# Kernel optimization log

Measured on AMD Instinct MI355X. Metric: run time of the kernel, lower is better.

The kernel has to match this reference:

```python
import jax, jax.numpy as jnp
import numpy as np

NEG_SLOPE = 0.2  # PyG GATConv default negative_slope


def gat_conv(x, edge_index, W, att_src, att_dst, bias):
    """PyG-style GATConv (concat heads, add_self_loops=True, eval mode).
    x: [N, F_in], edge_index: [2, E] (row 0 = src j, row 1 = dst i).
    W: [F_in, H*C], att_src/att_dst: [H, C], bias: [H*C].
    """
    N = x.shape[0]
    H, C = att_src.shape
    loops = jnp.arange(N, dtype=edge_index.dtype)
    src = jnp.concatenate([edge_index[0], loops])  # [E+N]
    dst = jnp.concatenate([edge_index[1], loops])
    h = (x @ W).reshape(N, H, C)                              # [N,H,C]
    a_src = jnp.einsum('nhc,hc->nh', h, att_src)              # [N,H]
    a_dst = jnp.einsum('nhc,hc->nh', h, att_dst)
    alpha = jax.nn.leaky_relu(a_src[src] + a_dst[dst], NEG_SLOPE)  # [E+N,H]
    # segment softmax over edges sharing the same destination node
    m = jax.ops.segment_max(alpha, dst, num_segments=N)       # [N,H]
    e = jnp.exp(alpha - jax.lax.stop_gradient(m)[dst])
    denom = jax.ops.segment_sum(e, dst, num_segments=N)       # [N,H]
    a = e / (denom[dst] + 1e-16)                              # [E+N,H]
    msg = h[src] * a[:, :, None]                              # [E+N,H,C]
    out = jax.ops.segment_sum(msg, dst, num_segments=N)       # [N,H,C]
    return out.reshape(N, H * C) + bias


def setup_inputs() -> dict:
    key = jax.random.key(0)
    ks = jax.random.split(key, 10)
    N, F, NC, C1, H1 = 50000, 128, 40, 16, 8
    E = 800000
    x = jax.random.normal(ks[0], (N, F), dtype=jnp.float32)
    edge_index = jax.random.randint(ks[1], (2, E), 0, N, dtype=jnp.int64)
    s1 = 1.0 / np.sqrt(F)
    W1 = jax.random.uniform(ks[2], (F, H1 * C1), jnp.float32, -s1, s1)
    att_src1 = jax.random.uniform(ks[3], (H1, C1), jnp.float32, -1.0, 1.0) * s1
    att_dst1 = jax.random.uniform(ks[4], (H1, C1), jnp.float32, -1.0, 1.0) * s1
    bias1 = jnp.zeros((H1 * C1,), jnp.float32)
    s2 = 1.0 / np.sqrt(H1 * C1)
    W2 = jax.random.uniform(ks[5], (H1 * C1, NC), jnp.float32, -s2, s2)
    att_src2 = jax.random.uniform(ks[6], (1, NC), jnp.float32, -1.0, 1.0) * s2
    att_dst2 = jax.random.uniform(ks[7], (1, NC), jnp.float32, -1.0, 1.0) * s2
    bias2 = jnp.zeros((NC,), jnp.float32)
    return {"x": x, "edge_index": edge_index, "W1": W1, "att_src1": att_src1,
            "att_dst1": att_dst1, "bias1": bias1, "W2": W2, "att_src2": att_src2,
            "att_dst2": att_dst2, "bias2": bias2}


def reference(x, edge_index, W1, att_src1, att_dst1, bias1, W2, att_src2, att_dst2, bias2):
    h = gat_conv(x, edge_index, W1, att_src1, att_dst1, bias1)   # [N, 128]
    # dropout in eval mode = identity
    out = gat_conv(h, edge_index, W2, att_src2, att_dst2, bias2)  # [N, 40]
    return out
```

## Files before the change

kernel.cpp:

```cpp
#include <hip/hip_runtime.h>
#include <hip/hip_bf16.h>
#include <math.h>

#define NEG_SLOPE 0.2f

typedef __bf16 bf16x8 __attribute__((ext_vector_type(8)));
typedef float f32x4 __attribute__((ext_vector_type(4)));

__device__ __forceinline__ float lrelu(float x) { return x > 0.f ? x : NEG_SLOPE * x; }

__device__ __forceinline__ unsigned short f2bfu(float f) {
    unsigned int ua = __float_as_uint(f);
    return (unsigned short)((ua + 0x7fffu + ((ua >> 16) & 1u)) >> 16);
}
__device__ __forceinline__ float bfu2f(unsigned short u) {
    return __uint_as_float(((unsigned int)u) << 16);
}
__device__ __forceinline__ float bf_lo(unsigned int u) { return __uint_as_float(u << 16); }
__device__ __forceinline__ float bf_hi(unsigned int u) { return __uint_as_float(u & 0xffff0000u); }

__global__ __launch_bounds__(256) void k_prep(const float* __restrict__ W1,
                                              bf16x8* __restrict__ Wp,
                                              const float* __restrict__ W2,
                                              bf16x8* __restrict__ W2p,
                                              const float* __restrict__ att_s1,
                                              const float* __restrict__ att_d1,
                                              const float* __restrict__ att_s2,
                                              const float* __restrict__ att_d2,
                                              int* __restrict__ cnt, int N) {
    int g = blockIdx.x * 256 + threadIdx.x;
    if (g < 2048) {
        int n = g & 15, quad = (g >> 4) & 3, c = (g >> 6) & 3, ct = g >> 8;
        bf16x8 v;
#pragma unroll
        for (int j = 0; j < 8; ++j)
            v[j] = (__bf16)W1[(c * 32 + quad * 8 + j) * 128 + ct * 16 + n];
        Wp[g] = v;
    } else if (g < 2560) {
        int idx = g - 2048;
        int n = idx & 15, quad = (idx >> 4) & 3, c = (idx >> 6) & 3, t8 = idx >> 8;
        int h = n & 7;
        const float* av = (n < 8) ? att_s1 : att_d1;
        bf16x8 vv;
#pragma unroll
        for (int j = 0; j < 8; ++j) {
            int f = c * 32 + quad * 8 + j;
            float full = 0.f;
            for (int cc = 0; cc < 16; ++cc)
                full += W1[f * 128 + h * 16 + cc] * av[h * 16 + cc];
            __bf16 hi = (__bf16)full;
            vv[j] = t8 ? (__bf16)(full - (float)hi) : hi;
        }
        Wp[g] = vv;
    } else if (g < 3328) {
        int idx = g - 2560;
        int n = idx & 15, quad = (idx >> 4) & 3, c = (idx >> 6) & 3, ct = idx >> 8;
        int colc = ct * 16 + n;
        bf16x8 v;
        if (colc < 40) {
#pragma unroll
            for (int j = 0; j < 8; ++j)
                v[j] = (__bf16)W2[(c * 32 + quad * 8 + j) * 40 + colc];
        } else if (ct == 2 && n >= 8 && n < 12) {
            const float* av = (n & 1) ? att_d2 : att_s2;
#pragma unroll
            for (int j = 0; j < 8; ++j) {
                int f = c * 32 + quad * 8 + j;
                float full = 0.f;
                for (int cc = 0; cc < 40; ++cc) full += W2[f * 40 + cc] * av[cc];
                __bf16 hi = (__bf16)full;
                v[j] = (n >= 10) ? (__bf16)(full - (float)hi) : hi;
            }
        } else {
#pragma unroll
            for (int j = 0; j < 8; ++j) v[j] = (__bf16)0.f;
        }
        W2p[idx] = v;
    }
    if (g < N) cnt[g] = 0;
}

__global__ __launch_bounds__(256) void k_hist(const int* __restrict__ ei, int E, int N,
                                              int* __restrict__ cnt,
                                              unsigned short* __restrict__ rank) {
    int e = blockIdx.x * 256 + threadIdx.x;
    if (e >= E + N) return;
    int d = (e < E) ? ei[E + e] : (e - E);
    rank[e] = (unsigned short)atomicAdd(&cnt[d], 1);
}

__global__ __launch_bounds__(256) void k_scan_part(const int* __restrict__ cnt, int N,
                                                   int* __restrict__ psum) {
    __shared__ int sh[256];
    int t = threadIdx.x;
    int base = blockIdx.x * 1024 + t * 4;
    int tl = 0;
#pragma unroll
    for (int j = 0; j < 4; ++j) tl += (base + j < N) ? cnt[base + j] : 0;
    sh[t] = tl; __syncthreads();
    for (int off = 128; off > 0; off >>= 1) {
        if (t < off) sh[t] += sh[t + off];
        __syncthreads();
    }
    if (t == 0) psum[blockIdx.x] = sh[0];
}

__global__ __launch_bounds__(256) void k_scan_add(const int* __restrict__ cnt, int N,
                                                  const int* __restrict__ psum,
                                                  int* __restrict__ rowptr) {
    __shared__ int sh[256];
    __shared__ int basep;
    int t = threadIdx.x;
    if (t == 0) {
        int s = 0;
        for (int i = 0; i < blockIdx.x; ++i) s += psum[i];
        basep = s;
    }
    int base = blockIdx.x * 1024 + t * 4;
    int c[4]; int tl = 0;
#pragma unroll
    for (int j = 0; j < 4; ++j) { c[j] = (base + j < N) ? cnt[base + j] : 0; tl += c[j]; }
    sh[t] = tl; __syncthreads();
    for (int off = 1; off < 256; off <<= 1) {
        int a = (t >= off) ? sh[t - off] : 0;
        __syncthreads();
        sh[t] += a;
        __syncthreads();
    }
    int run = basep + (sh[t] - tl);
#pragma unroll
    for (int j = 0; j < 4; ++j) {
        if (base + j < N) { rowptr[base + j] = run; run += c[j]; }
    }
}

__global__ __launch_bounds__(256) void k_scatter(const int* __restrict__ ei, int E, int N,
                                                 const int* __restrict__ rowptr,
                                                 const unsigned short* __restrict__ rank,
                                                 unsigned short* __restrict__ col) {
    int e = blockIdx.x * 256 + threadIdx.x;
    if (e >= E + N) return;
    int s, d;
    if (e < E) { s = ei[e]; d = ei[E + e]; } else { s = d = e - E; }
    col[rowptr[d] + (int)rank[e]] = (unsigned short)s;
}

__global__ __launch_bounds__(256) void k_ev1(const int* __restrict__ rowptr,
                                             const unsigned short* __restrict__ col,
                                             const float* __restrict__ a_src,
                                             const float* __restrict__ a_dst,
                                             float* __restrict__ evA,
                                             float* __restrict__ evB,
                                             unsigned short* __restrict__ d16,
                                             int N, int EN) {
    int slot = blockIdx.x * 256 + threadIdx.x;
    if (slot >= EN) return;
    int lo = 0, hi = N - 1;
    while (lo < hi) {
        int mid = (lo + hi + 1) >> 1;
        if (rowptr[mid] <= slot) lo = mid; else hi = mid - 1;
    }
    int d = lo;
    int s = (int)col[slot];
    d16[slot] = (unsigned short)d;
    float4 asA = *(const float4*)&a_src[(size_t)s * 8];
    float4 asB = *(const float4*)&a_src[(size_t)s * 8 + 4];
    float4 adA = *(const float4*)&a_dst[(size_t)d * 8];
    float4 adB = *(const float4*)&a_dst[(size_t)d * 8 + 4];
    float4 eA = make_float4(__expf(lrelu(asA.x + adA.x)), __expf(lrelu(asA.y + adA.y)),
                            __expf(lrelu(asA.z + adA.z)), __expf(lrelu(asA.w + adA.w)));
    float4 eB = make_float4(__expf(lrelu(asB.x + adB.x)), __expf(lrelu(asB.y + adB.y)),
                            __expf(lrelu(asB.z + adB.z)), __expf(lrelu(asB.w + adB.w)));
    *(float4*)&evA[(size_t)slot * 4] = eA;
    *(float4*)&evB[(size_t)slot * 4] = eB;
}

__global__ __launch_bounds__(256) void k_ev2(const unsigned short* __restrict__ col,
                                             const unsigned short* __restrict__ d16,
                                             const float* __restrict__ a_src2,
                                             const float* __restrict__ a_dst2,
                                             float* __restrict__ ev2, int EN) {
    int slot = blockIdx.x * 256 + threadIdx.x;
    if (slot >= EN) return;
    int s = (int)col[slot];
    int d = (int)d16[slot];
    ev2[slot] = __expf(lrelu(a_src2[s] + a_dst2[d]));
}

__global__ __launch_bounds__(256) void k_gemm1(const float* __restrict__ x,
                                               const bf16x8* __restrict__ Wp,
                                               unsigned short* __restrict__ h1A,
                                               unsigned short* __restrict__ h1B,
                                               float* __restrict__ a_src,
                                               float* __restrict__ a_dst, int N) {
    int t = threadIdx.x;
    int w = t >> 6, lane = t & 63, quad = lane >> 4, n16 = lane & 15;
    int row0 = blockIdx.x * 64 + w * 16;
    int arow = row0 + n16; if (arow >= N) arow = N - 1;
    const float* px = x + (size_t)arow * 128;

    bf16x8 ah[4], al[4];
#pragma unroll
    for (int c = 0; c < 4; ++c) {
        float4 v0 = *(const float4*)&px[c * 32 + quad * 8];
        float4 v1 = *(const float4*)&px[c * 32 + quad * 8 + 4];
        float xf[8] = {v0.x, v0.y, v0.z, v0.w, v1.x, v1.y, v1.z, v1.w};
#pragma unroll
        for (int j = 0; j < 8; ++j) {
            __bf16 hi = (__bf16)xf[j];
            ah[c][j] = hi;
            al[c][j] = (__bf16)(xf[j] - (float)hi);
        }
    }

    f32x4 acc[10];
#pragma unroll
    for (int ct = 0; ct < 10; ++ct) acc[ct] = (f32x4){0.f, 0.f, 0.f, 0.f};

    const uint4* wp4 = (const uint4*)Wp;
#pragma unroll
    for (int ct = 0; ct < 10; ++ct) {
#pragma unroll
        for (int c = 0; c < 4; ++c) {
            union { uint4 u; bf16x8 b; } bu;
            bu.u = wp4[((ct * 4 + c) * 4 + quad) * 16 + n16];
            acc[ct] = __builtin_amdgcn_mfma_f32_16x16x32_bf16(ah[c], bu.b, acc[ct], 0, 0, 0);
            acc[ct] = __builtin_amdgcn_mfma_f32_16x16x32_bf16(al[c], bu.b, acc[ct], 0, 0, 0);
        }
    }

    int nodeb = row0 + quad * 4;
#pragma unroll
    for (int ct = 0; ct < 8; ++ct) {
        unsigned short* hp = (ct < 4) ? h1A : h1B;
        int chl = (ct & 3) * 16 + n16;
#pragma unroll
        for (int reg = 0; reg < 4; ++reg) {
            int node = nodeb + reg;
            if (node < N) hp[(size_t)node * 64 + chl] = f2bfu(acc[ct][reg]);
        }
    }
#pragma unroll
    for (int reg = 0; reg < 4; ++reg) {
        int node = nodeb + reg;
        float av = acc[8][reg] + acc[9][reg];
        if (node < N) {
            if (n16 < 8) a_src[(size_t)node * 8 + n16] = av;
            else         a_dst[(size_t)node * 8 + (n16 - 8)] = av;
        }
    }
}

__global__ __launch_bounds__(256) void k_aggr1(const int* __restrict__ rowptr,
                                               const int* __restrict__ cnt,
                                               const unsigned short* __restrict__ col,
                                               const float* __restrict__ evA,
                                               const float* __restrict__ evB,
                                               const unsigned int* __restrict__ h1A,
                                               const unsigned int* __restrict__ h1B,
                                               const float* __restrict__ bias1,
                                               unsigned int* __restrict__ out1h,
                                               unsigned int* __restrict__ out1l,
                                               int N, int nag) {
    __shared__ float evs[4][2][128];
    __shared__ int   cls[4][2][32];
    int p = (blockIdx.x >= nag) ? 1 : 0;
    int blk = blockIdx.x - p * nag;
    const uint4* hp4 = (const uint4*)(p ? h1B : h1A);
    const float4* evp = (const float4*)(p ? evB : evA);
    int t = threadIdx.x;
    int w = t >> 6;
    int lane = t & 63;
    int half = lane >> 5;
    int u = lane & 31;
    int e4 = u >> 3;
    int v  = u & 7;
    int hh = v >> 1;
    int node = blk * 8 + w * 2 + half;
    bool nv = (node < N);
    int nodec = nv ? node : (N - 1);
    int beg = rowptr[nodec];
    int deg = nv ? cnt[nodec] : 0;
    int degO = __shfl_xor(deg, 32);
    int degmax = (deg > degO) ? deg : degO;
    if (degmax <= 0) return;

    float* myev = &evs[w][half][0];
    int*   mycl = &cls[w][half][0];

    float den = 0.f;
    float nm[8];
#pragma unroll
    for (int k = 0; k < 8; ++k) nm[k] = 0.f;

    int c = 0;
    while (c < degmax) {
        int slot = c + u;
        int slotc = (slot < deg) ? slot : (deg - 1);
        if (slotc < 0) slotc = 0;
        int su = (int)col[beg + slotc];
        float4 e4v = evp[beg + slotc];
        if (slot >= deg) e4v = make_float4(0.f, 0.f, 0.f, 0.f);
        *(float4*)&myev[u * 4] = e4v;
        mycl[u] = su;

        int ccm = degmax - c; ccm = (ccm < 32) ? ccm : 32;
        int ng = (ccm + 3) >> 2;
        int gl = ng - 1;
        int g1 = (1 < gl) ? 1 : gl;
        int g2 = (2 < gl) ? 2 : gl;
        int g3 = (3 < gl) ? 3 : gl;
        uint4 U0 = hp4[mycl[e4] * 8 + v];
        uint4 U1 = hp4[mycl[g1 * 4 + e4] * 8 + v];
        uint4 U2 = hp4[mycl[g2 * 4 + e4] * 8 + v];
        uint4 U3 = hp4[mycl[g3 * 4 + e4] * 8 + v];
        int body = ng - 4;
        int g = 0;
#pragma unroll 2
        for (; g < body; ++g) {
            uint4 UN = hp4[mycl[(g + 4) * 4 + e4] * 8 + v];
            float ev = myev[(g * 4 + e4) * 4 + hh];
            den += ev;
            nm[0] = fmaf(ev, bf_lo(U0.x), nm[0]);
            nm[1] = fmaf(ev, bf_hi(U0.x), nm[1]);
            nm[2] = fmaf(ev, bf_lo(U0.y), nm[2]);
            nm[3] = fmaf(ev, bf_hi(U0.y), nm[3]);
            nm[4] = fmaf(ev, bf_lo(U0.z), nm[4]);
            nm[5] = fmaf(ev, bf_hi(U0.z), nm[5]);
            nm[6] = fmaf(ev, bf_lo(U0.w), nm[6]);
            nm[7] = fmaf(ev, bf_hi(U0.w), nm[7]);
            U0 = U1; U1 = U2; U2 = U3; U3 = UN;
        }
        for (; g < ng; ++g) {
            float ev = myev[(g * 4 + e4) * 4 + hh];
            den += ev;
            nm[0] = fmaf(ev, bf_lo(U0.x), nm[0]);
            nm[1] = fmaf(ev, bf_hi(U0.x), nm[1]);
            nm[2] = fmaf(ev, bf_lo(U0.y), nm[2]);
            nm[3] = fmaf(ev, bf_hi(U0.y), nm[3]);
            nm[4] = fmaf(ev, bf_lo(U0.z), nm[4]);
            nm[5] = fmaf(ev, bf_hi(U0.z), nm[5]);
            nm[6] = fmaf(ev, bf_lo(U0.w), nm[6]);
            nm[7] = fmaf(ev, bf_hi(U0.w), nm[7]);
            U0 = U1; U1 = U2; U2 = U3;
        }
        c += 32;
    }
    den += __shfl_xor(den, 8);
    den += __shfl_xor(den, 16);
#pragma unroll
    for (int k = 0; k < 8; ++k) {
        nm[k] += __shfl_xor(nm[k], 8);
        nm[k] += __shfl_xor(nm[k], 16);
    }
    if (nv && e4 == 0) {
        float inv = 1.f / (den + 1e-16f);
        float4 b0 = *(const float4*)&bias1[p * 64 + v * 8];
        float4 b1 = *(const float4*)&bias1[p * 64 + v * 8 + 4];
        float bb[8] = {b0.x, b0.y, b0.z, b0.w, b1.x, b1.y, b1.z, b1.w};
        unsigned int H[4], L[4];
#pragma unroll
        for (int q = 0; q < 4; ++q) {
            float o0 = fmaf(nm[2 * q],     inv, bb[2 * q]);
            float o1 = fmaf(nm[2 * q + 1], inv, bb[2 * q + 1]);
            unsigned short h0 = f2bfu(o0), h1 = f2bfu(o1);
            float l0 = o0 - bfu2f(h0), l1 = o1 - bfu2f(h1);
            H[q] = (unsigned int)h0 | ((unsigned int)h1 << 16);
            L[q] = (unsigned int)f2bfu(l0) | ((unsigned int)f2bfu(l1) << 16);
        }
        size_t idx = (size_t)node * 64 + p * 32 + v * 4;
        *(uint4*)&out1h[idx] = make_uint4(H[0], H[1], H[2], H[3]);
        *(uint4*)&out1l[idx] = make_uint4(L[0], L[1], L[2], L[3]);
    }
}

__global__ __launch_bounds__(256) void k_gemm2(const unsigned int* __restrict__ out1h,
                                               const unsigned int* __restrict__ out1l,
                                               const bf16x8* __restrict__ W2p,
                                               unsigned short* __restrict__ h2s,
                                               float* __restrict__ a_src2,
                                               float* __restrict__ a_dst2, int N) {
    int t = threadIdx.x;
    int w = t >> 6, lane = t & 63, quad = lane >> 4, n16 = lane & 15;
    int row0 = blockIdx.x * 64 + w * 16;
    int arow = row0 + n16; if (arow >= N) arow = N - 1;

    bf16x8 ah[4], al[4];
#pragma unroll
    for (int c = 0; c < 4; ++c) {
        size_t base = (size_t)arow * 64 + (c * 32 + quad * 8) / 2;
        union { uint4 u; bf16x8 b; } hu, lu;
        hu.u = *(const uint4*)&out1h[base];
        lu.u = *(const uint4*)&out1l[base];
        ah[c] = hu.b;
        al[c] = lu.b;
    }

    f32x4 acc[3];
#pragma unroll
    for (int ct = 0; ct < 3; ++ct) acc[ct] = (f32x4){0.f, 0.f, 0.f, 0.f};

    const uint4* wp4 = (const uint4*)W2p;
#pragma unroll
    for (int ct = 0; ct < 3; ++ct) {
#pragma unroll
        for (int c = 0; c < 4; ++c) {
            union { uint4 u; bf16x8 b; } bu;
            bu.u = wp4[((ct * 4 + c) * 4 + quad) * 16 + n16];
            acc[ct] = __builtin_amdgcn_mfma_f32_16x16x32_bf16(ah[c], bu.b, acc[ct], 0, 0, 0);
            acc[ct] = __builtin_amdgcn_mfma_f32_16x16x32_bf16(al[c], bu.b, acc[ct], 0, 0, 0);
        }
    }

    int nodeb = row0 + quad * 4;
#pragma unroll
    for (int reg = 0; reg < 4; ++reg) {
        int node = nodeb + reg;
#pragma unroll
        for (int ct = 0; ct < 3; ++ct) {
            int ch = ct * 16 + n16;
            if (node < N && ch < 40) h2s[(size_t)node * 64 + ch] = f2bfu(acc[ct][reg]);
        }
        float fv = acc[2][reg];
        float fused = fv + __shfl_xor(fv, 2);
        if (node < N) {
            if (n16 == 8) a_src2[node] = fused;
            else if (n16 == 9) a_dst2[node] = fused;
        }
    }
}

__global__ __launch_bounds__(256) void k_aggr2(const int* __restrict__ rowptr,
                                               const int* __restrict__ cnt,
                                               const unsigned short* __restrict__ col,
                                               const float* __restrict__ ev2,
                                               const unsigned int* __restrict__ h2b,
                                               const float* __restrict__ bias2,
                                               float* __restrict__ out, int N) {
    __shared__ float evs[4][2][32];
    __shared__ int   cls[4][2][32];
    int t = threadIdx.x;
    int w = t >> 6;
    int lane = t & 63;
    int half = lane >> 5;
    int u = lane & 31;
    int e4 = u >> 3;
    int v  = u & 7;
    int node = blockIdx.x * 8 + w * 2 + half;
    bool nv = (node < N);
    int nodec = nv ? node : (N - 1);
    int beg = rowptr[nodec];
    int deg = nv ? cnt[nodec] : 0;
    int degO = __shfl_xor(deg, 32);
    int degmax = (deg > degO) ? deg : degO;
    if (degmax <= 0) return;

    const uint4* h24 = (const uint4*)h2b;
    float* myev = &evs[w][half][0];
    int*   mycl = &cls[w][half][0];

    float den = 0.f;
    float am[8];
#pragma unroll
    for (int k = 0; k < 8; ++k) am[k] = 0.f;

    int c = 0;
    while (c < degmax) {
        int slot = c + u;
        int slotc = (slot < deg) ? slot : (deg - 1);
        if (slotc < 0) slotc = 0;
        int su = (int)col[beg + slotc];
        float ev = ev2[beg + slotc];
        if (slot >= deg) ev = 0.f;
        myev[u] = ev;
        mycl[u] = su;

        int ccm = degmax - c; ccm = (ccm < 32) ? ccm : 32;
        int ng = (ccm + 3) >> 2;
        int gl = ng - 1;
        int g1 = (1 < gl) ? 1 : gl;
        int g2 = (2 < gl) ? 2 : gl;
        int g3 = (3 < gl) ? 3 : gl;
        uint4 U0 = h24[mycl[e4] * 8 + v];
        uint4 U1 = h24[mycl[g1 * 4 + e4] * 8 + v];
        uint4 U2 = h24[mycl[g2 * 4 + e4] * 8 + v];
        uint4 U3 = h24[mycl[g3 * 4 + e4] * 8 + v];
        int body = ng - 4;
        int g = 0;
#pragma unroll 2
        for (; g < body; ++g) {
            uint4 UN = h24[mycl[(g + 4) * 4 + e4] * 8 + v];
            float evv = myev[g * 4 + e4];
            den += evv;
            am[0] = fmaf(evv, bf_lo(U0.x), am[0]);
            am[1] = fmaf(evv, bf_hi(U0.x), am[1]);
            am[2] = fmaf(evv, bf_lo(U0.y), am[2]);
            am[3] = fmaf(evv, bf_hi(U0.y), am[3]);
            am[4] = fmaf(evv, bf_lo(U0.z), am[4]);
            am[5] = fmaf(evv, bf_hi(U0.z), am[5]);
            am[6] = fmaf(evv, bf_lo(U0.w), am[6]);
            am[7] = fmaf(evv, bf_hi(U0.w), am[7]);
            U0 = U1; U1 = U2; U2 = U3; U3 = UN;
        }
        for (; g < ng; ++g) {
            float evv = myev[g * 4 + e4];
            den += evv;
            am[0] = fmaf(evv, bf_lo(U0.x), am[0]);
            am[1] = fmaf(evv, bf_hi(U0.x), am[1]);
            am[2] = fmaf(evv, bf_lo(U0.y), am[2]);
            am[3] = fmaf(evv, bf_hi(U0.y), am[3]);
            am[4] = fmaf(evv, bf_lo(U0.z), am[4]);
            am[5] = fmaf(evv, bf_hi(U0.z), am[5]);
            am[6] = fmaf(evv, bf_lo(U0.w), am[6]);
            am[7] = fmaf(evv, bf_hi(U0.w), am[7]);
            U0 = U1; U1 = U2; U2 = U3;
        }
        c += 32;
    }
    den += __shfl_xor(den, 8);
    den += __shfl_xor(den, 16);
#pragma unroll
    for (int k = 0; k < 8; ++k) {
        am[k] += __shfl_xor(am[k], 8);
        am[k] += __shfl_xor(am[k], 16);
    }
    if (nv && e4 == 0 && v < 5) {
        float inv = 1.f / (den + 1e-16f);
        float4 b0 = *(const float4*)&bias2[v * 8];
        float4 b1 = *(const float4*)&bias2[v * 8 + 4];
        float4 o0 = make_float4(fmaf(am[0], inv, b0.x), fmaf(am[1], inv, b0.y),
                                fmaf(am[2], inv, b0.z), fmaf(am[3], inv, b0.w));
        float4 o1 = make_float4(fmaf(am[4], inv, b1.x), fmaf(am[5], inv, b1.y),
                                fmaf(am[6], inv, b1.z), fmaf(am[7], inv, b1.w));
        size_t ob = (size_t)node * 40 + v * 8;
        *(float4*)&out[ob] = o0;
        *(float4*)&out[ob + 4] = o1;
    }
}

extern "C" void kernel_launch(void* const* d_in, const int* in_sizes, int n_in,
                              void* d_out, int out_size, void* d_ws, size_t ws_size,
                              hipStream_t stream) {
    const float* x   = (const float*)d_in[0];
    const int*   ei  = (const int*)d_in[1];
    const float* W1  = (const float*)d_in[2];
    const float* as1 = (const float*)d_in[3];
    const float* ad1 = (const float*)d_in[4];
    const float* b1  = (const float*)d_in[5];
    const float* W2  = (const float*)d_in[6];
    const float* as2 = (const float*)d_in[7];
    const float* ad2 = (const float*)d_in[8];
    const float* b2  = (const float*)d_in[9];

    int N = in_sizes[0] / 128;
    int E = in_sizes[1] / 2;
    int EN = E + N;
    size_t Np = (size_t)((N + 3) & ~3);
    size_t ENp = ((size_t)EN + 3) & ~3;

    float* ws = (float*)d_ws;
    unsigned int* out1h = (unsigned int*)ws; ws += Np * 64;
    unsigned int* out1l = (unsigned int*)ws; ws += Np * 64;
    unsigned int* h1A = (unsigned int*)ws; ws += Np * 32;
    unsigned int* h1Bp = (unsigned int*)ws; ws += Np * 32;
    unsigned int* h2b = (unsigned int*)ws; ws += Np * 32;
    float* a_src1  = ws; ws += Np * 8;
    float* a_dst1  = ws; ws += Np * 8;
    float* a_src2v = ws; ws += Np;
    float* a_dst2v = ws; ws += Np;
    float* evA = ws; ws += ENp * 4;
    float* evB = ws; ws += ENp * 4;
    float* ev2 = ws; ws += ENp;
    bf16x8* Wp  = (bf16x8*)ws; ws += 2560 * 4;
    bf16x8* W2p = (bf16x8*)ws; ws += 768 * 4;
    int* cnt    = (int*)ws; ws += Np;
    int* rowptr = (int*)ws; ws += Np;
    int* psum   = (int*)ws; ws += 256;
    unsigned short* col  = (unsigned short*)ws; ws += ENp / 2 + 4;
    unsigned short* rank = (unsigned short*)ws; ws += ENp / 2 + 4;
    unsigned short* d16  = (unsigned short*)ws; ws += ENp / 2 + 4;

    int nb = (N + 1023) / 1024;
    int npre = (N > 3328 ? N : 3328);

    k_prep<<<(npre + 255) / 256, 256, 0, stream>>>(W1, Wp, W2, W2p,
                                                   as1, ad1, as2, ad2, cnt, N);
    k_hist<<<(EN + 255) / 256, 256, 0, stream>>>(ei, E, N, cnt, rank);
    k_scan_part<<<nb, 256, 0, stream>>>(cnt, N, psum);
    k_scan_add<<<nb, 256, 0, stream>>>(cnt, N, psum, rowptr);
    k_scatter<<<(EN + 255) / 256, 256, 0, stream>>>(ei, E, N, rowptr, rank, col);

    k_gemm1<<<(N + 63) / 64, 256, 0, stream>>>(x, Wp,
                                               (unsigned short*)h1A, (unsigned short*)h1Bp,
                                               a_src1, a_dst1, N);
    k_ev1<<<(EN + 255) / 256, 256, 0, stream>>>(rowptr, col, a_src1, a_dst1,
                                                evA, evB, d16, N, EN);
    int nag = (N + 7) / 8;
    k_aggr1<<<2 * nag, 256, 0, stream>>>(rowptr, cnt, col, evA, evB,
                                         h1A, h1Bp, b1, out1h, out1l, N, nag);
    k_gemm2<<<(N + 63) / 64, 256, 0, stream>>>(out1h, out1l, W2p,
                                               (unsigned short*)h2b, a_src2v, a_dst2v, N);
    k_ev2<<<(EN + 255) / 256, 256, 0, stream>>>(col, d16, a_src2v, a_dst2v, ev2, EN);
    k_aggr2<<<nag, 256, 0, stream>>>(rowptr, cnt, col, ev2, h2b, b2, (float*)d_out, N);
}
```

Measured before the change: 245.2 us.

## Fuse edge attention computation into aggregation kernels with block-level edge windows

```diff
diff --git a/kernel.cpp b/kernel.cpp
--- a/kernel.cpp
+++ b/kernel.cpp
@@ -3,6 +3,7 @@
 #include <math.h>
 
 #define NEG_SLOPE 0.2f
+#define WSZ 512
 
 typedef __bf16 bf16x8 __attribute__((ext_vector_type(8)));
 typedef float f32x4 __attribute__((ext_vector_type(4)));
@@ -130,7 +131,10 @@
     int run = basep + (sh[t] - tl);
 #pragma unroll
     for (int j = 0; j < 4; ++j) {
-        if (base + j < N) { rowptr[base + j] = run; run += c[j]; }
+        if (base + j < N) {
+            rowptr[base + j] = run; run += c[j];
+            if (base + j == N - 1) rowptr[N] = run;
+        }
     }
 }
 
@@ -143,48 +147,6 @@
     int s, d;
     if (e < E) { s = ei[e]; d = ei[E + e]; } else { s = d = e - E; }
     col[rowptr[d] + (int)rank[e]] = (unsigned short)s;
-}
-
-__global__ __launch_bounds__(256) void k_ev1(const int* __restrict__ rowptr,
-                                             const unsigned short* __restrict__ col,
-                                             const float* __restrict__ a_src,
-                                             const float* __restrict__ a_dst,
-                                             float* __restrict__ evA,
-                                             float* __restrict__ evB,
-                                             unsigned short* __restrict__ d16,
-                                             int N, int EN) {
-    int slot = blockIdx.x * 256 + threadIdx.x;
-    if (slot >= EN) return;
-    int lo = 0, hi = N - 1;
-    while (lo < hi) {
-        int mid = (lo + hi + 1) >> 1;
-        if (rowptr[mid] <= slot) lo = mid; else hi = mid - 1;
-    }
-    int d = lo;
-    int s = (int)col[slot];
-    d16[slot] = (unsigned short)d;
-    float4 asA = *(const float4*)&a_src[(size_t)s * 8];
-    float4 asB = *(const float4*)&a_src[(size_t)s * 8 + 4];
-    float4 adA = *(const float4*)&a_dst[(size_t)d * 8];
-    float4 adB = *(const float4*)&a_dst[(size_t)d * 8 + 4];
-    float4 eA = make_float4(__expf(lrelu(asA.x + adA.x)), __expf(lrelu(asA.y + adA.y)),
-                            __expf(lrelu(asA.z + adA.z)), __expf(lrelu(asA.w + adA.w)));
-    float4 eB = make_float4(__expf(lrelu(asB.x + adB.x)), __expf(lrelu(asB.y + adB.y)),
-                            __expf(lrelu(asB.z + adB.z)), __expf(lrelu(asB.w + adB.w)));
-    *(float4*)&evA[(size_t)slot * 4] = eA;
-    *(float4*)&evB[(size_t)slot * 4] = eB;
-}
-
-__global__ __launch_bounds__(256) void k_ev2(const unsigned short* __restrict__ col,
-                                             const unsigned short* __restrict__ d16,
-                                             const float* __restrict__ a_src2,
-                                             const float* __restrict__ a_dst2,
-                                             float* __restrict__ ev2, int EN) {
-    int slot = blockIdx.x * 256 + threadIdx.x;
-    if (slot >= EN) return;
-    int s = (int)col[slot];
-    int d = (int)d16[slot];
-    ev2[slot] = __expf(lrelu(a_src2[s] + a_dst2[d]));
 }
 
 __global__ __launch_bounds__(256) void k_gemm1(const float* __restrict__ x,
@@ -252,99 +214,122 @@
 }
 
 __global__ __launch_bounds__(256) void k_aggr1(const int* __restrict__ rowptr,
-                                               const int* __restrict__ cnt,
                                                const unsigned short* __restrict__ col,
-                                               const float* __restrict__ evA,
-                                               const float* __restrict__ evB,
+                                               const float* __restrict__ a_src,
+                                               const float* __restrict__ a_dst,
                                                const unsigned int* __restrict__ h1A,
                                                const unsigned int* __restrict__ h1B,
                                                const float* __restrict__ bias1,
                                                unsigned int* __restrict__ out1h,
                                                unsigned int* __restrict__ out1l,
                                                int N, int nag) {
-    __shared__ float evs[4][2][128];
-    __shared__ int   cls[4][2][32];
+    __shared__ float4 evL[WSZ];
+    __shared__ int    colL[WSZ];
+    __shared__ int    rpL[9];
+    __shared__ float4 adL[8];
     int p = (blockIdx.x >= nag) ? 1 : 0;
     int blk = blockIdx.x - p * nag;
     const uint4* hp4 = (const uint4*)(p ? h1B : h1A);
-    const float4* evp = (const float4*)(p ? evB : evA);
     int t = threadIdx.x;
-    int w = t >> 6;
-    int lane = t & 63;
-    int half = lane >> 5;
-    int u = lane & 31;
-    int e4 = u >> 3;
-    int v  = u & 7;
-    int hh = v >> 1;
-    int node = blk * 8 + w * 2 + half;
+    int node0 = blk * 8;
+    if (t < 9) {
+        int nd = node0 + t; if (nd > N) nd = N;
+        rpL[t] = rowptr[nd];
+    }
+    if (t >= 64 && t < 72) {
+        int nd = node0 + (t - 64); if (nd >= N) nd = N - 1;
+        adL[t - 64] = *(const float4*)&a_dst[(size_t)nd * 8 + p * 4];
+    }
+    __syncthreads();
+    int w0v = rpL[0], end8 = rpL[8];
+
+    int w = t >> 6, lane = t & 63, half = lane >> 5, u = lane & 31;
+    int e4 = u >> 3, v = u & 7, hh = v >> 1;
+    int idx8 = w * 2 + half;
+    int node = node0 + idx8;
     bool nv = (node < N);
-    int nodec = nv ? node : (N - 1);
-    int beg = rowptr[nodec];
-    int deg = nv ? cnt[nodec] : 0;
-    int degO = __shfl_xor(deg, 32);
-    int degmax = (deg > degO) ? deg : degO;
-    if (degmax <= 0) return;
-
-    float* myev = &evs[w][half][0];
-    int*   mycl = &cls[w][half][0];
+    int beg = rpL[idx8], end = rpL[idx8 + 1];
 
     float den = 0.f;
     float nm[8];
 #pragma unroll
     for (int k = 0; k < 8; ++k) nm[k] = 0.f;
 
-    int c = 0;
-    while (c < degmax) {
-        int slot = c + u;
-        int slotc = (slot < deg) ? slot : (deg - 1);
-        if (slotc < 0) slotc = 0;
-        int su = (int)col[beg + slotc];
-        float4 e4v = evp[beg + slotc];
-        if (slot >= deg) e4v = make_float4(0.f, 0.f, 0.f, 0.f);
-        *(float4*)&myev[u * 4] = e4v;
-        mycl[u] = su;
-
-        int ccm = degmax - c; ccm = (ccm < 32) ? ccm : 32;
-        int ng = (ccm + 3) >> 2;
-        int gl = ng - 1;
-        int g1 = (1 < gl) ? 1 : gl;
-        int g2 = (2 < gl) ? 2 : gl;
-        int g3 = (3 < gl) ? 3 : gl;
-        uint4 U0 = hp4[mycl[e4] * 8 + v];
-        uint4 U1 = hp4[mycl[g1 * 4 + e4] * 8 + v];
-        uint4 U2 = hp4[mycl[g2 * 4 + e4] * 8 + v];
-        uint4 U3 = hp4[mycl[g3 * 4 + e4] * 8 + v];
-        int body = ng - 4;
-        int g = 0;
+    for (int w0 = w0v; w0 < end8; w0 += WSZ) {
+        int wend = w0 + WSZ; if (wend > end8) wend = end8;
+        int wsz = wend - w0;
+        if (w0 != w0v) __syncthreads();
+        for (int s = w0 + t; s < wend; s += 256) {
+            int su = (int)col[s];
+            int lo2 = 0;
+            if (rpL[lo2 + 4] <= s) lo2 += 4;
+            if (rpL[lo2 + 2] <= s) lo2 += 2;
+            if (rpL[lo2 + 1] <= s) lo2 += 1;
+            float4 as4 = *(const float4*)&a_src[(size_t)su * 8 + p * 4];
+            float4 ad4 = adL[lo2];
+            float4 e;
+            e.x = __expf(lrelu(as4.x + ad4.x));
+            e.y = __expf(lrelu(as4.y + ad4.y));
+            e.z = __expf(lrelu(as4.z + ad4.z));
+            e.w = __expf(lrelu(as4.w + ad4.w));
+            evL[s - w0] = e;
+            colL[s - w0] = su;
+        }
+        __syncthreads();
+        int lbeg = (beg > w0) ? beg : w0;
+        int lend = (end < wend) ? end : wend;
+        int ldeg = lend - lbeg;
+        int ldO = __shfl_xor(ldeg, 32);
+        int ldm = (ldeg > ldO) ? ldeg : ldO;
+        int ob0 = lbeg - w0;
+        const float* evf = (const float*)evL;
+        for (int c = 0; c < ldm; c += 32) {
+            int ccm = ldeg - c; ccm = (ccm < 32) ? ccm : 32;
+            int ng = (ccm + 3) >> 2;
+            int gl = ng - 1;
+            int g1 = (1 < gl) ? 1 : gl;
+            int g2 = (2 < gl) ? 2 : gl;
+            int g3 = (3 < gl) ? 3 : gl;
+            int ob = ob0 + c;
+#define CIDX(i) ({ int _x = ob + (i); _x = (_x < 0) ? 0 : _x; (_x >= wsz) ? (wsz - 1) : _x; })
+            uint4 U0 = hp4[colL[CIDX(e4)] * 8 + v];
+            uint4 U1 = hp4[colL[CIDX(g1 * 4 + e4)] * 8 + v];
+            uint4 U2 = hp4[colL[CIDX(g2 * 4 + e4)] * 8 + v];
+            uint4 U3 = hp4[colL[CIDX(g3 * 4 + e4)] * 8 + v];
+            int body = ng - 4;
+            int g = 0;
 #pragma unroll 2
-        for (; g < body; ++g) {
-            uint4 UN = hp4[mycl[(g + 4) * 4 + e4] * 8 + v];
-            float ev = myev[(g * 4 + e4) * 4 + hh];
-            den += ev;
-            nm[0] = fmaf(ev, bf_lo(U0.x), nm[0]);
-            nm[1] = fmaf(ev, bf_hi(U0.x), nm[1]);
-            nm[2] = fmaf(ev, bf_lo(U0.y), nm[2]);
-            nm[3] = fmaf(ev, bf_hi(U0.y), nm[3]);
-            nm[4] = fmaf(ev, bf_lo(U0.z), nm[4]);
-            nm[5] = fmaf(ev, bf_hi(U0.z), nm[5]);
-            nm[6] = fmaf(ev, bf_lo(U0.w), nm[6]);
-            nm[7] = fmaf(ev, bf_hi(U0.w), nm[7]);
-            U0 = U1; U1 = U2; U2 = U3; U3 = UN;
-        }
-        for (; g < ng; ++g) {
-            float ev = myev[(g * 4 + e4) * 4 + hh];
-            den += ev;
-            nm[0] = fmaf(ev, bf_lo(U0.x), nm[0]);
-            nm[1] = fmaf(ev, bf_hi(U0.x), nm[1]);
-            nm[2] = fmaf(ev, bf_lo(U0.y), nm[2]);
-            nm[3] = fmaf(ev, bf_hi(U0.y), nm[3]);
-            nm[4] = fmaf(ev, bf_lo(U0.z), nm[4]);
-            nm[5] = fmaf(ev, bf_hi(U0.z), nm[5]);
-            nm[6] = fmaf(ev, bf_lo(U0.w), nm[6]);
-            nm[7] = fmaf(ev, bf_hi(U0.w), nm[7]);
-            U0 = U1; U1 = U2; U2 = U3;
-        }
-        c += 32;
+            for (; g < body; ++g) {
+                uint4 UN = hp4[colL[CIDX((g + 4) * 4 + e4)] * 8 + v];
+                int ii = g * 4 + e4;
+                float ev = (c + ii < ldeg) ? evf[CIDX(ii) * 4 + hh] : 0.f;
+                den += ev;
+                nm[0] = fmaf(ev, bf_lo(U0.x), nm[0]);
+                nm[1] = fmaf(ev, bf_hi(U0.x), nm[1]);
+                nm[2] = fmaf(ev, bf_lo(U0.y), nm[2]);
+                nm[3] = fmaf(ev, bf_hi(U0.y), nm[3]);
+                nm[4] = fmaf(ev, bf_lo(U0.z), nm[4]);
+                nm[5] = fmaf(ev, bf_hi(U0.z), nm[5]);
+                nm[6] = fmaf(ev, bf_lo(U0.w), nm[6]);
+                nm[7] = fmaf(ev, bf_hi(U0.w), nm[7]);
+                U0 = U1; U1 = U2; U2 = U3; U3 = UN;
+            }
+            for (; g < ng; ++g) {
+                int ii = g * 4 + e4;
+                float ev = (c + ii < ldeg) ? evf[CIDX(ii) * 4 + hh] : 0.f;
+                den += ev;
+                nm[0] = fmaf(ev, bf_lo(U0.x), nm[0]);
+                nm[1] = fmaf(ev, bf_hi(U0.x), nm[1]);
+                nm[2] = fmaf(ev, bf_lo(U0.y), nm[2]);
+                nm[3] = fmaf(ev, bf_hi(U0.y), nm[3]);
+                nm[4] = fmaf(ev, bf_lo(U0.z), nm[4]);
+                nm[5] = fmaf(ev, bf_hi(U0.z), nm[5]);
+                nm[6] = fmaf(ev, bf_lo(U0.w), nm[6]);
+                nm[7] = fmaf(ev, bf_hi(U0.w), nm[7]);
+                U0 = U1; U1 = U2; U2 = U3;
+            }
+#undef CIDX
+        }
     }
     den += __shfl_xor(den, 8);
     den += __shfl_xor(den, 16);
@@ -431,91 +416,109 @@
 }
 
 __global__ __launch_bounds__(256) void k_aggr2(const int* __restrict__ rowptr,
-                                               const int* __restrict__ cnt,
                                                const unsigned short* __restrict__ col,
-                                               const float* __restrict__ ev2,
+                                               const float* __restrict__ a_src2,
+                                               const float* __restrict__ a_dst2,
                                                const unsigned int* __restrict__ h2b,
                                                const float* __restrict__ bias2,
                                                float* __restrict__ out, int N) {
-    __shared__ float evs[4][2][32];
-    __shared__ int   cls[4][2][32];
+    __shared__ float evL[WSZ];
+    __shared__ int   colL[WSZ];
+    __shared__ int   rpL[9];
+    __shared__ float adL[8];
     int t = threadIdx.x;
-    int w = t >> 6;
-    int lane = t & 63;
-    int half = lane >> 5;
-    int u = lane & 31;
-    int e4 = u >> 3;
-    int v  = u & 7;
-    int node = blockIdx.x * 8 + w * 2 + half;
+    int node0 = blockIdx.x * 8;
+    if (t < 9) {
+        int nd = node0 + t; if (nd > N) nd = N;
+        rpL[t] = rowptr[nd];
+    }
+    if (t >= 64 && t < 72) {
+        int nd = node0 + (t - 64); if (nd >= N) nd = N - 1;
+        adL[t - 64] = a_dst2[nd];
+    }
+    __syncthreads();
+    int w0v = rpL[0], end8 = rpL[8];
+
+    int w = t >> 6, lane = t & 63, half = lane >> 5, u = lane & 31;
+    int e4 = u >> 3, v = u & 7;
+    int idx8 = w * 2 + half;
+    int node = node0 + idx8;
     bool nv = (node < N);
-    int nodec = nv ? node : (N - 1);
-    int beg = rowptr[nodec];
-    int deg = nv ? cnt[nodec] : 0;
-    int degO = __shfl_xor(deg, 32);
-    int degmax = (deg > degO) ? deg : degO;
-    if (degmax <= 0) return;
+    int beg = rpL[idx8], end = rpL[idx8 + 1];
 
     const uint4* h24 = (const uint4*)h2b;
-    float* myev = &evs[w][half][0];
-    int*   mycl = &cls[w][half][0];
-
     float den = 0.f;
     float am[8];
 #pragma unroll
     for (int k = 0; k < 8; ++k) am[k] = 0.f;
 
-    int c = 0;
-    while (c < degmax) {
-        int slot = c + u;
-        int slotc = (slot < deg) ? slot : (deg - 1);
-        if (slotc < 0) slotc = 0;
-        int su = (int)col[beg + slotc];
-        float ev = ev2[beg + slotc];
-        if (slot >= deg) ev = 0.f;
-        myev[u] = ev;
-        mycl[u] = su;
-
-        int ccm = degmax - c; ccm = (ccm < 32) ? ccm : 32;
-        int ng = (ccm + 3) >> 2;
-        int gl = ng - 1;
-        int g1 = (1 < gl) ? 1 : gl;
-        int g2 = (2 < gl) ? 2 : gl;
-        int g3 = (3 < gl) ? 3 : gl;
-        uint4 U0 = h24[mycl[e4] * 8 + v];
-        uint4 U1 = h24[mycl[g1 * 4 + e4] * 8 + v];
-        uint4 U2 = h24[mycl[g2 * 4 + e4] * 8 + v];
-        uint4 U3 = h24[mycl[g3 * 4 + e4] * 8 + v];
-        int body = ng - 4;
-        int g = 0;
+    for (int w0 = w0v; w0 < end8; w0 += WSZ) {
+        int wend = w0 + WSZ; if (wend > end8) wend = end8;
+        int wsz = wend - w0;
+        if (w0 != w0v) __syncthreads();
+        for (int s = w0 + t; s < wend; s += 256) {
+            int su = (int)col[s];
+            int lo2 = 0;
+            if (rpL[lo2 + 4] <= s) lo2 += 4;
+            if (rpL[lo2 + 2] <= s) lo2 += 2;
+            if (rpL[lo2 + 1] <= s) lo2 += 1;
+            evL[s - w0] = __expf(lrelu(a_src2[su] + adL[lo2]));
+            colL[s - w0] = su;
+        }
+        __syncthreads();
+        int lbeg = (beg > w0) ? beg : w0;
+        int lend = (end < wend) ? end : wend;
+        int ldeg = lend - lbeg;
+        int ldO = __shfl_xor(ldeg, 32);
+        int ldm = (ldeg > ldO) ? ldeg : ldO;
+        int ob0 = lbeg - w0;
+        for (int c = 0; c < ldm; c += 32) {
+            int ccm = ldeg - c; ccm = (ccm < 32) ? ccm : 32;
+            int ng = (ccm + 3) >> 2;
+            int gl = ng - 1;
+            int g1 = (1 < gl) ? 1 : gl;
+            int g2 = (2 < gl) ? 2 : gl;
+            int g3 = (3 < gl) ? 3 : gl;
+            int ob = ob0 + c;
+#define CIDX(i) ({ int _x = ob + (i); _x = (_x < 0) ? 0 : _x; (_x >= wsz) ? (wsz - 1) : _x; })
+            uint4 U0 = h24[colL[CIDX(e4)] * 8 + v];
+            uint4 U1 = h24[colL[CIDX(g1 * 4 + e4)] * 8 + v];
+            uint4 U2 = h24[colL[CIDX(g2 * 4 + e4)] * 8 + v];
+            uint4 U3 = h24[colL[CIDX(g3 * 4 + e4)] * 8 + v];
+            int body = ng - 4;
+            int g = 0;
 #pragma unroll 2
-        for (; g < body; ++g) {
-            uint4 UN = h24[mycl[(g + 4) * 4 + e4] * 8 + v];
-            float evv = myev[g * 4 + e4];
-            den += evv;
-            am[0] = fmaf(evv, bf_lo(U0.x), am[0]);
-            am[1] = fmaf(evv, bf_hi(U0.x), am[1]);
-            am[2] = fmaf(evv, bf_lo(U0.y), am[2]);
-            am[3] = fmaf(evv, bf_hi(U0.y), am[3]);
-            am[4] = fmaf(evv, bf_lo(U0.z), am[4]);
-            am[5] = fmaf(evv, bf_hi(U0.z), am[5]);
-            am[6] = fmaf(evv, bf_lo(U0.w), am[6]);
-            am[7] = fmaf(evv, bf_hi(U0.w), am[7]);
-            U0 = U1; U1 = U2; U2 = U3; U3 = UN;
-        }
-        for (; g < ng; ++g) {
-            float evv = myev[g * 4 + e4];
-            den += evv;
-            am[0] = fmaf(evv, bf_lo(U0.x), am[0]);
-            am[1] = fmaf(evv, bf_hi(U0.x), am[1]);
-            am[2] = fmaf(evv, bf_lo(U0.y), am[2]);
-            am[3] = fmaf(evv, bf_hi(U0.y), am[3]);
-            am[4] = fmaf(evv, bf_lo(U0.z), am[4]);
-            am[5] = fmaf(evv, bf_hi(U0.z), am[5]);
-            am[6] = fmaf(evv, bf_lo(U0.w), am[6]);
-            am[7] = fmaf(evv, bf_hi(U0.w), am[7]);
-            U0 = U1; U1 = U2; U2 = U3;
-        }
-        c += 32;
+            for (; g < body; ++g) {
+                uint4 UN = h24[colL[CIDX((g + 4) * 4 + e4)] * 8 + v];
+                int ii = g * 4 + e4;
+                float evv = (c + ii < ldeg) ? evL[CIDX(ii)] : 0.f;
+                den += evv;
+                am[0] = fmaf(evv, bf_lo(U0.x), am[0]);
+                am[1] = fmaf(evv, bf_hi(U0.x), am[1]);
+                am[2] = fmaf(evv, bf_lo(U0.y), am[2]);
+                am[3] = fmaf(evv, bf_hi(U0.y), am[3]);
+                am[4] = fmaf(evv, bf_lo(U0.z), am[4]);
+                am[5] = fmaf(evv, bf_hi(U0.z), am[5]);
+                am[6] = fmaf(evv, bf_lo(U0.w), am[6]);
+                am[7] = fmaf(evv, bf_hi(U0.w), am[7]);
+                U0 = U1; U1 = U2; U2 = U3; U3 = UN;
+            }
+            for (; g < ng; ++g) {
+                int ii = g * 4 + e4;
+                float evv = (c + ii < ldeg) ? evL[CIDX(ii)] : 0.f;
+                den += evv;
+                am[0] = fmaf(evv, bf_lo(U0.x), am[0]);
+                am[1] = fmaf(evv, bf_hi(U0.x), am[1]);
+                am[2] = fmaf(evv, bf_lo(U0.y), am[2]);
+                am[3] = fmaf(evv, bf_hi(U0.y), am[3]);
+                am[4] = fmaf(evv, bf_lo(U0.z), am[4]);
+                am[5] = fmaf(evv, bf_hi(U0.z), am[5]);
+                am[6] = fmaf(evv, bf_lo(U0.w), am[6]);
+                am[7] = fmaf(evv, bf_hi(U0.w), am[7]);
+                U0 = U1; U1 = U2; U2 = U3;
+            }
+#undef CIDX
+        }
     }
     den += __shfl_xor(den, 8);
     den += __shfl_xor(den, 16);
@@ -568,38 +571,31 @@
     float* a_dst1  = ws; ws += Np * 8;
     float* a_src2v = ws; ws += Np;
     float* a_dst2v = ws; ws += Np;
-    float* evA = ws; ws += ENp * 4;
-    float* evB = ws; ws += ENp * 4;
-    float* ev2 = ws; ws += ENp;
     bf16x8* Wp  = (bf16x8*)ws; ws += 2560 * 4;
     bf16x8* W2p = (bf16x8*)ws; ws += 768 * 4;
     int* cnt    = (int*)ws; ws += Np;
-    int* rowptr = (int*)ws; ws += Np;
+    int* rowptr = (int*)ws; ws += Np + 4;
     int* psum   = (int*)ws; ws += 256;
     unsigned short* col  = (unsigned short*)ws; ws += ENp / 2 + 4;
     unsigned short* rank = (unsigned short*)ws; ws += ENp / 2 + 4;
-    unsigned short* d16  = (unsigned short*)ws; ws += ENp / 2 + 4;
 
     int nb = (N + 1023) / 1024;
     int npre = (N > 3328 ? N : 3328);
 
     k_prep<<<(npre + 255) / 256, 256, 0, stream>>>(W1, Wp, W2, W2p,
                                                    as1, ad1, as2, ad2, cnt, N);
+    k_gemm1<<<(N + 63) / 64, 256, 0, stream>>>(x, Wp,
+                                               (unsigned short*)h1A, (unsigned short*)h1Bp,
+                                               a_src1, a_dst1, N);
     k_hist<<<(EN + 255) / 256, 256, 0, stream>>>(ei, E, N, cnt, rank);
     k_scan_part<<<nb, 256, 0, stream>>>(cnt, N, psum);
     k_scan_add<<<nb, 256, 0, stream>>>(cnt, N, psum, rowptr);
     k_scatter<<<(EN + 255) / 256, 256, 0, stream>>>(ei, E, N, rowptr, rank, col);
 
-    k_gemm1<<<(N + 63) / 64, 256, 0, stream>>>(x, Wp,
-                                               (unsigned short*)h1A, (unsigned short*)h1Bp,
-                                               a_src1, a_dst1, N);
-    k_ev1<<<(EN + 255) / 256, 256, 0, stream>>>(rowptr, col, a_src1, a_dst1,
-                                                evA, evB, d16, N, EN);
     int nag = (N + 7) / 8;
-    k_aggr1<<<2 * nag, 256, 0, stream>>>(rowptr, cnt, col, evA, evB,
+    k_aggr1<<<2 * nag, 256, 0, stream>>>(rowptr, col, a_src1, a_dst1,
                                          h1A, h1Bp, b1, out1h, out1l, N, nag);
     k_gemm2<<<(N + 63) / 64, 256, 0, stream>>>(out1h, out1l, W2p,
                                                (unsigned short*)h2b, a_src2v, a_dst2v, N);
-    k_ev2<<<(EN + 255) / 256, 256, 0, stream>>>(col, d16, a_src2v, a_dst2v, ev2, EN);
-    k_aggr2<<<nag, 256, 0, stream>>>(rowptr, cnt, col, ev2, h2b, b2, (float*)d_out, N);
-}
+    k_aggr2<<<nag, 256, 0, stream>>>(rowptr, col, a_src2v, a_dst2v, h2b, b2, (float*)d_out, N);
+}
```

Result: faster. 235.8 us (-3.8%).

## Fuse edge-score computation into aggregation kernels and restructure aggr1 per-lane gather

Applied to the files above, without the earlier changes.

```diff
diff --git a/kernel.cpp b/kernel.cpp
--- a/kernel.cpp
+++ b/kernel.cpp
@@ -145,48 +145,6 @@
     col[rowptr[d] + (int)rank[e]] = (unsigned short)s;
 }
 
-__global__ __launch_bounds__(256) void k_ev1(const int* __restrict__ rowptr,
-                                             const unsigned short* __restrict__ col,
-                                             const float* __restrict__ a_src,
-                                             const float* __restrict__ a_dst,
-                                             float* __restrict__ evA,
-                                             float* __restrict__ evB,
-                                             unsigned short* __restrict__ d16,
-                                             int N, int EN) {
-    int slot = blockIdx.x * 256 + threadIdx.x;
-    if (slot >= EN) return;
-    int lo = 0, hi = N - 1;
-    while (lo < hi) {
-        int mid = (lo + hi + 1) >> 1;
-        if (rowptr[mid] <= slot) lo = mid; else hi = mid - 1;
-    }
-    int d = lo;
-    int s = (int)col[slot];
-    d16[slot] = (unsigned short)d;
-    float4 asA = *(const float4*)&a_src[(size_t)s * 8];
-    float4 asB = *(const float4*)&a_src[(size_t)s * 8 + 4];
-    float4 adA = *(const float4*)&a_dst[(size_t)d * 8];
-    float4 adB = *(const float4*)&a_dst[(size_t)d * 8 + 4];
-    float4 eA = make_float4(__expf(lrelu(asA.x + adA.x)), __expf(lrelu(asA.y + adA.y)),
-                            __expf(lrelu(asA.z + adA.z)), __expf(lrelu(asA.w + adA.w)));
-    float4 eB = make_float4(__expf(lrelu(asB.x + adB.x)), __expf(lrelu(asB.y + adB.y)),
-                            __expf(lrelu(asB.z + adB.z)), __expf(lrelu(asB.w + adB.w)));
-    *(float4*)&evA[(size_t)slot * 4] = eA;
-    *(float4*)&evB[(size_t)slot * 4] = eB;
-}
-
-__global__ __launch_bounds__(256) void k_ev2(const unsigned short* __restrict__ col,
-                                             const unsigned short* __restrict__ d16,
-                                             const float* __restrict__ a_src2,
-                                             const float* __restrict__ a_dst2,
-                                             float* __restrict__ ev2, int EN) {
-    int slot = blockIdx.x * 256 + threadIdx.x;
-    if (slot >= EN) return;
-    int s = (int)col[slot];
-    int d = (int)d16[slot];
-    ev2[slot] = __expf(lrelu(a_src2[s] + a_dst2[d]));
-}
-
 __global__ __launch_bounds__(256) void k_gemm1(const float* __restrict__ x,
                                                const bf16x8* __restrict__ Wp,
                                                unsigned short* __restrict__ h1A,
@@ -254,8 +212,8 @@
 __global__ __launch_bounds__(256) void k_aggr1(const int* __restrict__ rowptr,
                                                const int* __restrict__ cnt,
                                                const unsigned short* __restrict__ col,
-                                               const float* __restrict__ evA,
-                                               const float* __restrict__ evB,
+                                               const float* __restrict__ a_src,
+                                               const float* __restrict__ a_dst,
                                                const unsigned int* __restrict__ h1A,
                                                const unsigned int* __restrict__ h1B,
                                                const float* __restrict__ bias1,
@@ -266,16 +224,12 @@
     __shared__ int   cls[4][2][32];
     int p = (blockIdx.x >= nag) ? 1 : 0;
     int blk = blockIdx.x - p * nag;
-    const uint4* hp4 = (const uint4*)(p ? h1B : h1A);
-    const float4* evp = (const float4*)(p ? evB : evA);
+    const unsigned int* hp = p ? h1B : h1A;
     int t = threadIdx.x;
     int w = t >> 6;
     int lane = t & 63;
     int half = lane >> 5;
     int u = lane & 31;
-    int e4 = u >> 3;
-    int v  = u & 7;
-    int hh = v >> 1;
     int node = blk * 8 + w * 2 + half;
     bool nv = (node < N);
     int nodec = nv ? node : (N - 1);
@@ -285,92 +239,69 @@
     int degmax = (deg > degO) ? deg : degO;
     if (degmax <= 0) return;
 
+    int hh = u >> 3;
+    float4 ad4 = *(const float4*)&a_dst[(size_t)nodec * 8 + p * 4];
+
     float* myev = &evs[w][half][0];
     int*   mycl = &cls[w][half][0];
 
-    float den = 0.f;
-    float nm[8];
-#pragma unroll
-    for (int k = 0; k < 8; ++k) nm[k] = 0.f;
-
+    float den = 0.f, n0 = 0.f, n1 = 0.f;
     int c = 0;
     while (c < degmax) {
         int slot = c + u;
         int slotc = (slot < deg) ? slot : (deg - 1);
         if (slotc < 0) slotc = 0;
         int su = (int)col[beg + slotc];
-        float4 e4v = evp[beg + slotc];
-        if (slot >= deg) e4v = make_float4(0.f, 0.f, 0.f, 0.f);
-        *(float4*)&myev[u * 4] = e4v;
+        float4 as4 = *(const float4*)&a_src[(size_t)su * 8 + p * 4];
+        bool valid = (slot < deg);
+        float e0 = valid ? __expf(lrelu(as4.x + ad4.x)) : 0.f;
+        float e1 = valid ? __expf(lrelu(as4.y + ad4.y)) : 0.f;
+        float e2 = valid ? __expf(lrelu(as4.z + ad4.z)) : 0.f;
+        float e3 = valid ? __expf(lrelu(as4.w + ad4.w)) : 0.f;
+        *(float4*)&myev[u * 4] = make_float4(e0, e1, e2, e3);
         mycl[u] = su;
 
         int ccm = degmax - c; ccm = (ccm < 32) ? ccm : 32;
-        int ng = (ccm + 3) >> 2;
-        int gl = ng - 1;
-        int g1 = (1 < gl) ? 1 : gl;
-        int g2 = (2 < gl) ? 2 : gl;
-        int g3 = (3 < gl) ? 3 : gl;
-        uint4 U0 = hp4[mycl[e4] * 8 + v];
-        uint4 U1 = hp4[mycl[g1 * 4 + e4] * 8 + v];
-        uint4 U2 = hp4[mycl[g2 * 4 + e4] * 8 + v];
-        uint4 U3 = hp4[mycl[g3 * 4 + e4] * 8 + v];
-        int body = ng - 4;
-        int g = 0;
-#pragma unroll 2
-        for (; g < body; ++g) {
-            uint4 UN = hp4[mycl[(g + 4) * 4 + e4] * 8 + v];
-            float ev = myev[(g * 4 + e4) * 4 + hh];
+        int last = ccm - 1;
+        int s0 = mycl[0];
+        unsigned int u0 = hp[s0 * 32 + u];
+        int i1 = (1 < last) ? 1 : last;
+        int s1 = mycl[i1];
+        unsigned int u1 = hp[s1 * 32 + u];
+        int i2 = (2 < last) ? 2 : last;
+        int s2 = mycl[i2];
+        unsigned int u2 = hp[s2 * 32 + u];
+        int body = ccm - 3;
+        int i = 0;
+#pragma unroll 4
+        for (; i < body; ++i) {
+            int sN = mycl[i + 3];
+            unsigned int uN = hp[sN * 32 + u];
+            float ev = myev[i * 4 + hh];
             den += ev;
-            nm[0] = fmaf(ev, bf_lo(U0.x), nm[0]);
-            nm[1] = fmaf(ev, bf_hi(U0.x), nm[1]);
-            nm[2] = fmaf(ev, bf_lo(U0.y), nm[2]);
-            nm[3] = fmaf(ev, bf_hi(U0.y), nm[3]);
-            nm[4] = fmaf(ev, bf_lo(U0.z), nm[4]);
-            nm[5] = fmaf(ev, bf_hi(U0.z), nm[5]);
-            nm[6] = fmaf(ev, bf_lo(U0.w), nm[6]);
-            nm[7] = fmaf(ev, bf_hi(U0.w), nm[7]);
-            U0 = U1; U1 = U2; U2 = U3; U3 = UN;
-        }
-        for (; g < ng; ++g) {
-            float ev = myev[(g * 4 + e4) * 4 + hh];
+            n0 = fmaf(ev, bf_lo(u0), n0);
+            n1 = fmaf(ev, bf_hi(u0), n1);
+            u0 = u1; u1 = u2; u2 = uN;
+        }
+        for (; i < ccm; ++i) {
+            float ev = myev[i * 4 + hh];
             den += ev;
-            nm[0] = fmaf(ev, bf_lo(U0.x), nm[0]);
-            nm[1] = fmaf(ev, bf_hi(U0.x), nm[1]);
-            nm[2] = fmaf(ev, bf_lo(U0.y), nm[2]);
-            nm[3] = fmaf(ev, bf_hi(U0.y), nm[3]);
-            nm[4] = fmaf(ev, bf_lo(U0.z), nm[4]);
-            nm[5] = fmaf(ev, bf_hi(U0.z), nm[5]);
-            nm[6] = fmaf(ev, bf_lo(U0.w), nm[6]);
-            nm[7] = fmaf(ev, bf_hi(U0.w), nm[7]);
-            U0 = U1; U1 = U2; U2 = U3;
+            n0 = fmaf(ev, bf_lo(u0), n0);
+            n1 = fmaf(ev, bf_hi(u0), n1);
+            u0 = u1; u1 = u2;
         }
         c += 32;
     }
-    den += __shfl_xor(den, 8);
-    den += __shfl_xor(den, 16);
-#pragma unroll
-    for (int k = 0; k < 8; ++k) {
-        nm[k] += __shfl_xor(nm[k], 8);
-        nm[k] += __shfl_xor(nm[k], 16);
-    }
-    if (nv && e4 == 0) {
+    if (nv) {
         float inv = 1.f / (den + 1e-16f);
-        float4 b0 = *(const float4*)&bias1[p * 64 + v * 8];
-        float4 b1 = *(const float4*)&bias1[p * 64 + v * 8 + 4];
-        float bb[8] = {b0.x, b0.y, b0.z, b0.w, b1.x, b1.y, b1.z, b1.w};
-        unsigned int H[4], L[4];
-#pragma unroll
-        for (int q = 0; q < 4; ++q) {
-            float o0 = fmaf(nm[2 * q],     inv, bb[2 * q]);
-            float o1 = fmaf(nm[2 * q + 1], inv, bb[2 * q + 1]);
-            unsigned short h0 = f2bfu(o0), h1 = f2bfu(o1);
-            float l0 = o0 - bfu2f(h0), l1 = o1 - bfu2f(h1);
-            H[q] = (unsigned int)h0 | ((unsigned int)h1 << 16);
-            L[q] = (unsigned int)f2bfu(l0) | ((unsigned int)f2bfu(l1) << 16);
-        }
-        size_t idx = (size_t)node * 64 + p * 32 + v * 4;
-        *(uint4*)&out1h[idx] = make_uint4(H[0], H[1], H[2], H[3]);
-        *(uint4*)&out1l[idx] = make_uint4(L[0], L[1], L[2], L[3]);
+        int ch = p * 64 + 2 * u;
+        float2 b = *(const float2*)&bias1[ch];
+        float o0 = fmaf(n0, inv, b.x), o1 = fmaf(n1, inv, b.y);
+        unsigned short h0 = f2bfu(o0), h1 = f2bfu(o1);
+        float l0 = o0 - bfu2f(h0), l1 = o1 - bfu2f(h1);
+        size_t idx = (size_t)node * 64 + p * 32 + u;
+        out1h[idx] = (unsigned int)h0 | ((unsigned int)h1 << 16);
+        out1l[idx] = (unsigned int)f2bfu(l0) | ((unsigned int)f2bfu(l1) << 16);
     }
 }
 
@@ -433,7 +364,8 @@
 __global__ __launch_bounds__(256) void k_aggr2(const int* __restrict__ rowptr,
                                                const int* __restrict__ cnt,
                                                const unsigned short* __restrict__ col,
-                                               const float* __restrict__ ev2,
+                                               const float* __restrict__ a_src,
+                                               const float* __restrict__ a_dst,
                                                const unsigned int* __restrict__ h2b,
                                                const float* __restrict__ bias2,
                                                float* __restrict__ out, int N) {
@@ -456,6 +388,7 @@
     if (degmax <= 0) return;
 
     const uint4* h24 = (const uint4*)h2b;
+    float ad = a_dst[nodec];
     float* myev = &evs[w][half][0];
     int*   mycl = &cls[w][half][0];
 
@@ -470,8 +403,7 @@
         int slotc = (slot < deg) ? slot : (deg - 1);
         if (slotc < 0) slotc = 0;
         int su = (int)col[beg + slotc];
-        float ev = ev2[beg + slotc];
-        if (slot >= deg) ev = 0.f;
+        float ev = (slot < deg) ? __expf(lrelu(a_src[su] + ad)) : 0.f;
         myev[u] = ev;
         mycl[u] = su;
 
@@ -568,38 +500,31 @@
     float* a_dst1  = ws; ws += Np * 8;
     float* a_src2v = ws; ws += Np;
     float* a_dst2v = ws; ws += Np;
-    float* evA = ws; ws += ENp * 4;
-    float* evB = ws; ws += ENp * 4;
-    float* ev2 = ws; ws += ENp;
     bf16x8* Wp  = (bf16x8*)ws; ws += 2560 * 4;
     bf16x8* W2p = (bf16x8*)ws; ws += 768 * 4;
     int* cnt    = (int*)ws; ws += Np;
-    int* rowptr = (int*)ws; ws += Np;
+    int* rowptr = (int*)ws; ws += Np + 4;
     int* psum   = (int*)ws; ws += 256;
     unsigned short* col  = (unsigned short*)ws; ws += ENp / 2 + 4;
     unsigned short* rank = (unsigned short*)ws; ws += ENp / 2 + 4;
-    unsigned short* d16  = (unsigned short*)ws; ws += ENp / 2 + 4;
 
     int nb = (N + 1023) / 1024;
     int npre = (N > 3328 ? N : 3328);
 
     k_prep<<<(npre + 255) / 256, 256, 0, stream>>>(W1, Wp, W2, W2p,
                                                    as1, ad1, as2, ad2, cnt, N);
+    k_gemm1<<<(N + 63) / 64, 256, 0, stream>>>(x, Wp,
+                                               (unsigned short*)h1A, (unsigned short*)h1Bp,
+                                               a_src1, a_dst1, N);
     k_hist<<<(EN + 255) / 256, 256, 0, stream>>>(ei, E, N, cnt, rank);
     k_scan_part<<<nb, 256, 0, stream>>>(cnt, N, psum);
     k_scan_add<<<nb, 256, 0, stream>>>(cnt, N, psum, rowptr);
     k_scatter<<<(EN + 255) / 256, 256, 0, stream>>>(ei, E, N, rowptr, rank, col);
 
-    k_gemm1<<<(N + 63) / 64, 256, 0, stream>>>(x, Wp,
-                                               (unsigned short*)h1A, (unsigned short*)h1Bp,
-                                               a_src1, a_dst1, N);
-    k_ev1<<<(EN + 255) / 256, 256, 0, stream>>>(rowptr, col, a_src1, a_dst1,
-                                                evA, evB, d16, N, EN);
     int nag = (N + 7) / 8;
-    k_aggr1<<<2 * nag, 256, 0, stream>>>(rowptr, cnt, col, evA, evB,
+    k_aggr1<<<2 * nag, 256, 0, stream>>>(rowptr, cnt, col, a_src1, a_dst1,
                                          h1A, h1Bp, b1, out1h, out1l, N, nag);
     k_gemm2<<<(N + 63) / 64, 256, 0, stream>>>(out1h, out1l, W2p,
                                                (unsigned short*)h2b, a_src2v, a_dst2v, N);
-    k_ev2<<<(EN + 255) / 256, 256, 0, stream>>>(col, d16, a_src2v, a_dst2v, ev2, EN);
-    k_aggr2<<<nag, 256, 0, stream>>>(rowptr, cnt, col, ev2, h2b, b2, (float*)d_out, N);
-}
+    k_aggr2<<<nag, 256, 0, stream>>>(rowptr, cnt, col, a_src2v, a_dst2v, h2b, b2, (float*)d_out, N);
+}
```

Result: faster. 232.8 us (-5.0%).
